# Kernel tuning notes

Measured on AMD Instinct MI355X. Metric: run time of the kernel, lower is better.

Reference implementation:

```python
import jax, jax.numpy as jnp
import numpy as np

N, E, K = 10000, 160000, 5
K3 = K ** 3  # 125 spline kernel entries (kernel_size=5, dim=3)
NUM_CLASSES = 6890
# 8 corner combinations of the degree-1 open B-spline in 3 dims
_COMBOS = jnp.asarray(np.array([[i, j, k] for i in (0, 1) for j in (0, 1) for k in (0, 1)], dtype=np.int32))


def spline_basis(pseudo):
    # pseudo: [E,3] in [0,1]; degree-1 open B-spline, kernel_size K per dim
    p = pseudo * (K - 1)
    lo_f = jnp.floor(p)
    frac = p - lo_f                                   # [E,3]
    lo = jnp.clip(lo_f.astype(jnp.int32), 0, K - 1)    # [E,3]
    hi = jnp.minimum(lo + 1, K - 1)
    w = jnp.stack([1.0 - frac, frac], axis=-1)         # [E,3,2]
    idx = jnp.stack([lo, hi], axis=-1)                 # [E,3,2]
    c = _COMBOS                                        # [8,3]
    b = w[:, 0, c[:, 0]] * w[:, 1, c[:, 1]] * w[:, 2, c[:, 2]]          # [E,8]
    flat = idx[:, 0, c[:, 0]] + K * idx[:, 1, c[:, 1]] + K * K * idx[:, 2, c[:, 2]]  # [E,8]
    return b, flat


def spline_conv(x, src, dst, b, flat, W, root, bias):
    # x: [N,in], W: [K3,in,out], root: [in,out], bias: [out]
    xW = jnp.einsum('ni,kio->nko', x, W)               # [N,K3,out]
    gathered = xW[src[:, None], flat]                  # [E,8,out]
    msg = jnp.einsum('es,eso->eo', b, gathered)        # [E,out]
    agg = jax.ops.segment_sum(msg, dst, num_segments=N)
    deg = jax.ops.segment_sum(jnp.ones((msg.shape[0],), msg.dtype), dst, num_segments=N)
    agg = agg / jnp.maximum(deg, 1.0)[:, None]         # mean aggregation
    return agg + x @ root + bias


def setup_inputs() -> dict:
    key = jax.random.key(0)
    ks = jax.random.split(key, 24)
    s = 0.1
    x = jax.random.normal(ks[0], (N, 1), jnp.float32)
    edge_index = jax.random.randint(ks[1], (2, E), 0, N)
    pseudo = jax.random.uniform(ks[2], (E, 3), dtype=jnp.float32)
    W1 = jax.random.normal(ks[3], (K3, 1, 32), jnp.float32) * s
    root1 = jax.random.normal(ks[4], (1, 32), jnp.float32) * s
    b1 = jnp.zeros((32,), jnp.float32)
    W2 = jax.random.normal(ks[5], (K3, 32, 64), jnp.float32) * s
    root2 = jax.random.normal(ks[6], (32, 64), jnp.float32) * s
    b2 = jnp.zeros((64,), jnp.float32)
    Ws = jax.random.normal(ks[7], (4, K3, 64, 64), jnp.float32) * s  # convs 3-6
    roots = jax.random.normal(ks[8], (4, 64, 64), jnp.float32) * s
    bs = jnp.zeros((4, 64), jnp.float32)
    lin1_w = jax.random.normal(ks[9], (64, 256), jnp.float32) * s
    lin1_b = jnp.zeros((256,), jnp.float32)
    lin2_w = jax.random.normal(ks[10], (256, NUM_CLASSES), jnp.float32) * s
    lin2_b = jnp.zeros((NUM_CLASSES,), jnp.float32)
    return {'x': x, 'edge_index': edge_index, 'pseudo': pseudo,
            'W1': W1, 'root1': root1, 'b1': b1,
            'W2': W2, 'root2': root2, 'b2': b2,
            'Ws': Ws, 'roots': roots, 'bs': bs,
            'lin1_w': lin1_w, 'lin1_b': lin1_b, 'lin2_w': lin2_w, 'lin2_b': lin2_b}


def reference(x, edge_index, pseudo, W1, root1, b1, W2, root2, b2, Ws, roots, bs,
              lin1_w, lin1_b, lin2_w, lin2_b):
    src, dst = edge_index[0], edge_index[1]
    b, flat = spline_basis(pseudo)
    h = jax.nn.elu(spline_conv(x, src, dst, b, flat, W1, root1, b1))
    h = jax.nn.elu(spline_conv(h, src, dst, b, flat, W2, root2, b2))
    for l in range(4):  # convs 3-6, fixed layer loop
        h = jax.nn.elu(spline_conv(h, src, dst, b, flat, Ws[l], roots[l], bs[l]))
    h = jax.nn.elu(h @ lin1_w + lin1_b)
    # dropout is identity in eval mode
    logits = h @ lin2_w + lin2_b
    return jax.nn.log_softmax(logits, axis=-1)
```

## Files before the change

kernel.cpp:

```cpp
#include <hip/hip_runtime.h>
#include <hip/hip_bf16.h>
#include <math.h>

#define Nn 10000
#define Ee 160000
#define NPB 40
#define NBLK 250
#define NKER 125
#define NBUCK (NBLK * NKER)
#define KCHUNK 32

#define MPAD 10048
#define NPAD 6912
#define NCLS 6890

typedef short bf16x8 __attribute__((ext_vector_type(8)));
typedef float f32x4  __attribute__((ext_vector_type(4)));

__global__ __launch_bounds__(256) void basis_kernel(const float* __restrict__ pseudo,
                                                    float* __restrict__ bw,
                                                    int* __restrict__ fl)
{
    int e = blockIdx.x * 256 + threadIdx.x;
    if (e >= Ee) return;
    float p0 = pseudo[e * 3 + 0] * 4.f;
    float p1 = pseudo[e * 3 + 1] * 4.f;
    float p2 = pseudo[e * 3 + 2] * 4.f;
    float f0 = floorf(p0), f1 = floorf(p1), f2 = floorf(p2);
    float fr0 = p0 - f0, fr1 = p1 - f1, fr2 = p2 - f2;
    int lo0 = (int)f0; lo0 = lo0 < 0 ? 0 : (lo0 > 4 ? 4 : lo0);
    int lo1 = (int)f1; lo1 = lo1 < 0 ? 0 : (lo1 > 4 ? 4 : lo1);
    int lo2 = (int)f2; lo2 = lo2 < 0 ? 0 : (lo2 > 4 ? 4 : lo2);
    int hi0 = lo0 + 1 > 4 ? 4 : lo0 + 1;
    int hi1 = lo1 + 1 > 4 ? 4 : lo1 + 1;
    int hi2 = lo2 + 1 > 4 ? 4 : lo2 + 1;
#pragma unroll
    for (int s = 0; s < 8; ++s) {
        int c0 = (s >> 2) & 1, c1 = (s >> 1) & 1, c2 = s & 1;
        float b = (c0 ? fr0 : 1.f - fr0) * (c1 ? fr1 : 1.f - fr1) * (c2 ? fr2 : 1.f - fr2);
        int f = (c0 ? hi0 : lo0) + 5 * (c1 ? hi1 : lo1) + 25 * (c2 ? hi2 : lo2);
        bw[e * 8 + s] = b;
        fl[e * 8 + s] = f;
    }
}

__global__ __launch_bounds__(256) void deg_kernel(const int* __restrict__ dst, int* __restrict__ degi)
{
    int e = blockIdx.x * 256 + threadIdx.x;
    if (e >= Ee) return;
    atomicAdd(&degi[dst[e]], 1);
}

__global__ __launch_bounds__(256) void invdeg_kernel(const int* __restrict__ degi, float* __restrict__ invdeg)
{
    int n = blockIdx.x * 256 + threadIdx.x;
    if (n >= Nn) return;
    int d = degi[n];
    invdeg[n] = 1.f / (float)(d > 0 ? d : 1);
}

__global__ __launch_bounds__(256) void hist_kernel(const int* __restrict__ dst, const int* __restrict__ fl,
                                                   int* __restrict__ hist)
{
    int t = blockIdx.x * 256 + threadIdx.x;
    if (t >= Ee * 8) return;
    int e = t >> 3;
    int key = (dst[e] / NPB) * NKER + fl[t];
    atomicAdd(&hist[key], 1);
}

__global__ __launch_bounds__(1024) void scan_kernel(const int* __restrict__ hist, int* __restrict__ boff)
{
    const int T = 1024;
    const int per = (NBUCK + T - 1) / T;
    int t = threadIdx.x;
    int beg = t * per;
    int end = beg + per; if (end > NBUCK) end = NBUCK;
    int s = 0;
    for (int i = beg; i < end && i < NBUCK; ++i) s += hist[i];
    __shared__ int tmp[1024];
    tmp[t] = s;
    __syncthreads();
    for (int o2 = 1; o2 < 1024; o2 <<= 1) {
        int v = (t >= o2) ? tmp[t - o2] : 0;
        __syncthreads();
        tmp[t] += v;
        __syncthreads();
    }
    int run = tmp[t] - s;
    for (int i = beg; i < end && i < NBUCK; ++i) { boff[i] = run; run += hist[i]; }
    if (t == T - 1) boff[NBUCK] = run;
}

__global__ __launch_bounds__(256) void fill_kernel(const int* __restrict__ srcA, const int* __restrict__ dstA,
                                                   const float* __restrict__ bw, const int* __restrict__ fl,
                                                   int* __restrict__ cursor, uint2* __restrict__ recs)
{
    int t = blockIdx.x * 256 + threadIdx.x;
    if (t >= Ee * 8) return;
    int e = t >> 3;
    int d = dstA[e];
    int key = (d / NPB) * NKER + fl[t];
    int pos = atomicAdd(&cursor[key], 1);
    unsigned meta = (unsigned)srcA[e] | ((unsigned)(d % NPB) << 16);
    recs[pos] = make_uint2(meta, __float_as_uint(bw[t]));
}

template <int CIN, int COUT>
__global__ __launch_bounds__(256) void conv_pairs_kernel(const uint2* __restrict__ recs,
                                                         const int* __restrict__ boff,
                                                         const float* __restrict__ xin,
                                                         const float* __restrict__ W,
                                                         float* __restrict__ agg)
{
    __shared__ float aggl[NPB * COUT];
    const int blk = blockIdx.x;
    for (int idx = threadIdx.x; idx < NPB * COUT; idx += 256) aggl[idx] = 0.f;
    __syncthreads();

    const int lane = threadIdx.x & 63;
    const int wid  = threadIdx.x >> 6;
    const int o    = lane;

    int k0 = blockIdx.y * KCHUNK;
    int k1 = k0 + KCHUNK; if (k1 > NKER) k1 = NKER;

    for (int k = k0 + wid; k < k1; k += 4) {
        int bidx = blk * NKER + k;
        int pb = boff[bidx], pe = boff[bidx + 1];
        if (pb >= pe) continue;
        float wreg[CIN];
#pragma unroll
        for (int i = 0; i < CIN; ++i)
            wreg[i] = (o < COUT) ? W[(k * CIN + i) * COUT + o] : 0.f;

        for (int p = pb; p < pe; ++p) {
            uint2 r = recs[p];
            unsigned meta = (unsigned)__builtin_amdgcn_readfirstlane((int)r.x);
            float wt = __uint_as_float(r.y);
            int src = (int)(meta & 0xFFFFu);
            int dl  = (int)(meta >> 16);
            const float* xs = xin + src * CIN;
            float m0 = 0.f, m1 = 0.f, m2 = 0.f, m3 = 0.f;
            if (CIN >= 4) {
#pragma unroll
                for (int i = 0; i < CIN; i += 4) {
                    m0 += xs[i + 0] * wreg[i + 0];
                    m1 += xs[i + 1] * wreg[i + 1];
                    m2 += xs[i + 2] * wreg[i + 2];
                    m3 += xs[i + 3] * wreg[i + 3];
                }
            } else {
#pragma unroll
                for (int i = 0; i < CIN; ++i) m0 += xs[i] * wreg[i];
            }
            float m = (m0 + m1) + (m2 + m3);
            if (o < COUT) atomicAdd(&aggl[dl * COUT + o], wt * m);
        }
    }
    __syncthreads();
    for (int idx = threadIdx.x; idx < NPB * COUT; idx += 256) {
        int n = blk * NPB + idx / COUT;
        if (n < Nn) atomicAdd(&agg[n * COUT + (idx % COUT)], aggl[idx]);
    }
}

template <int CIN, int COUT>
__global__ __launch_bounds__(256) void epilogue_kernel(const float* __restrict__ agg,
                                                       const float* __restrict__ xin,
                                                       const float* __restrict__ root,
                                                       const float* __restrict__ bias,
                                                       const float* __restrict__ invdeg,
                                                       float* __restrict__ out)
{
    int idx = blockIdx.x * 256 + threadIdx.x;
    int n = idx / COUT, o = idx % COUT;
    if (n >= Nn) return;
    float r0 = 0.f, r1 = 0.f;
#pragma unroll
    for (int i = 0; i < CIN; i += 2) {
        r0 += xin[n * CIN + i] * root[i * COUT + o];
        if (CIN > 1) r1 += xin[n * CIN + i + 1] * root[(i + 1) * COUT + o];
    }
    float v = agg[n * COUT + o] * invdeg[n] + r0 + r1 + bias[o];
    out[n * COUT + o] = v > 0.f ? v : expm1f(v);
}

__global__ __launch_bounds__(256) void lin1_kernel(const float* __restrict__ h,
                                                   const float* __restrict__ w1,
                                                   const float* __restrict__ b1,
                                                   __hip_bfloat16* __restrict__ out)
{
    int n = blockIdx.x;
    __shared__ float hl[64];
    if (threadIdx.x < 64) hl[threadIdx.x] = h[n * 64 + threadIdx.x];
    __syncthreads();
    int j = threadIdx.x;
    float a0 = b1[j], a1 = 0.f, a2 = 0.f, a3 = 0.f;
#pragma unroll
    for (int i = 0; i < 64; i += 4) {
        a0 += hl[i + 0] * w1[(i + 0) * 256 + j];
        a1 += hl[i + 1] * w1[(i + 1) * 256 + j];
        a2 += hl[i + 2] * w1[(i + 2) * 256 + j];
        a3 += hl[i + 3] * w1[(i + 3) * 256 + j];
    }
    float acc = (a0 + a1) + (a2 + a3);
    float v = acc > 0.f ? acc : expm1f(acc);
    out[(size_t)n * 256 + j] = __float2bfloat16(v);
}

__global__ __launch_bounds__(256) void w2t_kernel(const float* __restrict__ w2,
                                                  __hip_bfloat16* __restrict__ w2t)
{
    __shared__ float t[32][33];
    int n0 = blockIdx.x * 32;
    int k0 = blockIdx.y * 32;
    int tx = threadIdx.x & 31, ty = threadIdx.x >> 5;
#pragma unroll
    for (int q = 0; q < 4; ++q) {
        int k = k0 + ty + 8 * q, n = n0 + tx;
        t[ty + 8 * q][tx] = (n < NCLS) ? w2[(size_t)k * NCLS + n] : 0.f;
    }
    __syncthreads();
#pragma unroll
    for (int q = 0; q < 4; ++q) {
        int n = n0 + ty + 8 * q;
        w2t[(size_t)n * 256 + k0 + tx] = __float2bfloat16(t[tx][ty + 8 * q]);
    }
}

__global__ __launch_bounds__(256) void lin2_mfma_kernel(const __hip_bfloat16* __restrict__ hbf,
                                                        const __hip_bfloat16* __restrict__ w2t,
                                                        const float* __restrict__ b2,
                                                        float* __restrict__ out)
{
    const int tid  = threadIdx.x;
    const int lane = tid & 63, wid = tid >> 6;
    const int wr = wid & 1, wc = wid >> 1;
    const int quad = lane >> 4, lq = lane & 15;

    const int mbase = blockIdx.x * 64 + wr * 32;
    const int nbase = blockIdx.y * 128 + wc * 64;

    f32x4 acc[2][4];
#pragma unroll
    for (int i = 0; i < 2; ++i)
#pragma unroll
        for (int j = 0; j < 4; ++j) acc[i][j] = (f32x4){0.f, 0.f, 0.f, 0.f};

    const unsigned short* A = (const unsigned short*)hbf;
    const unsigned short* B = (const unsigned short*)w2t;

    for (int kc = 0; kc < 256; kc += 32) {
        bf16x8 af[2], bfr[4];
#pragma unroll
        for (int mt = 0; mt < 2; ++mt)
            af[mt] = *(const bf16x8*)(A + (size_t)(mbase + mt * 16 + lq) * 256 + kc + quad * 8);
#pragma unroll
        for (int nt = 0; nt < 4; ++nt)
            bfr[nt] = *(const bf16x8*)(B + (size_t)(nbase + nt * 16 + lq) * 256 + kc + quad * 8);
#pragma unroll
        for (int mt = 0; mt < 2; ++mt)
#pragma unroll
            for (int nt = 0; nt < 4; ++nt)
                acc[mt][nt] = __builtin_amdgcn_mfma_f32_16x16x32_bf16(af[mt], bfr[nt], acc[mt][nt], 0, 0, 0);
    }

#pragma unroll
    for (int nt = 0; nt < 4; ++nt) {
        int col = nbase + nt * 16 + lq;
        if (col >= NCLS) continue;
        float bb = b2[col];
#pragma unroll
        for (int mt = 0; mt < 2; ++mt) {
#pragma unroll
            for (int r = 0; r < 4; ++r) {
                int row = mbase + mt * 16 + quad * 4 + r;
                if (row < Nn) out[(size_t)row * NCLS + col] = acc[mt][nt][r] + bb;
            }
        }
    }
}

__global__ __launch_bounds__(1024) void lsm_kernel(float* __restrict__ out)
{
    int row = blockIdx.x;
    float* p = out + (size_t)row * NCLS;
    __shared__ float red[16];
    int tid = threadIdx.x, lane = tid & 63, wid = tid >> 6;

    float m = -3.4e38f;
    for (int jj = tid; jj < NCLS; jj += 1024) m = fmaxf(m, p[jj]);
#pragma unroll
    for (int off = 32; off > 0; off >>= 1) m = fmaxf(m, __shfl_down(m, off));
    if (lane == 0) red[wid] = m;
    __syncthreads();
    if (tid == 0) {
        float mm = red[0];
        for (int w = 1; w < 16; ++w) mm = fmaxf(mm, red[w]);
        red[0] = mm;
    }
    __syncthreads();
    m = red[0];
    __syncthreads();

    float s = 0.f;
    for (int jj = tid; jj < NCLS; jj += 1024) s += expf(p[jj] - m);
#pragma unroll
    for (int off = 32; off > 0; off >>= 1) s += __shfl_down(s, off);
    if (lane == 0) red[wid] = s;
    __syncthreads();
    if (tid == 0) {
        float ss = 0.f;
        for (int w = 1; w < 16; ++w) ss += red[w];
        red[0] += ss;
    }
    __syncthreads();
    float lse = m + logf(red[0]);
    for (int jj = tid; jj < NCLS; jj += 1024) p[jj] -= lse;
}

extern "C" void kernel_launch(void* const* d_in, const int* in_sizes, int n_in,
                              void* d_out, int out_size, void* d_ws, size_t ws_size,
                              hipStream_t stream)
{
    const float* x      = (const float*)d_in[0];
    const int*   ei     = (const int*)d_in[1];
    const float* pseudo = (const float*)d_in[2];
    const float* W1     = (const float*)d_in[3];
    const float* root1  = (const float*)d_in[4];
    const float* b1     = (const float*)d_in[5];
    const float* W2     = (const float*)d_in[6];
    const float* root2  = (const float*)d_in[7];
    const float* b2     = (const float*)d_in[8];
    const float* Ws     = (const float*)d_in[9];
    const float* roots  = (const float*)d_in[10];
    const float* bs     = (const float*)d_in[11];
    const float* l1w    = (const float*)d_in[12];
    const float* l1b    = (const float*)d_in[13];
    const float* l2w    = (const float*)d_in[14];
    const float* l2b    = (const float*)d_in[15];
    float* out = (float*)d_out;

    const int* srcA = ei;
    const int* dstA = ei + Ee;

    char* base = (char*)d_ws;
    size_t off = 0;
    auto carve = [&](size_t bytes) -> void* {
        void* p = base + off;
        off += (bytes + 255) & ~(size_t)255;
        return p;
    };
    float* bw     = (float*)carve((size_t)Ee * 8 * 4);
    int*   fl     = (int*)carve((size_t)Ee * 8 * 4);
    int*   hist   = (int*)carve((size_t)NBUCK * 4);
    int*   boff   = (int*)carve((size_t)(NBUCK + 1) * 4);
    int*   cursor = (int*)carve((size_t)NBUCK * 4);
    uint2* recs   = (uint2*)carve((size_t)Ee * 8 * 8);
    int*   degi   = (int*)carve((size_t)Nn * 4);
    float* invdeg = (float*)carve((size_t)Nn * 4);
    float* agg    = (float*)carve((size_t)Nn * 64 * 4);
    float* hA     = (float*)carve((size_t)Nn * 64 * 4);
    float* hB     = (float*)carve((size_t)Nn * 64 * 4);
    __hip_bfloat16* hbf = (__hip_bfloat16*)carve((size_t)MPAD * 256 * 2);
    __hip_bfloat16* w2t = (__hip_bfloat16*)carve((size_t)NPAD * 256 * 2);
    (void)ws_size; (void)n_in; (void)in_sizes; (void)out_size;

    hipMemsetAsync(hist, 0, (size_t)NBUCK * 4, stream);
    hipMemsetAsync(degi, 0, (size_t)Nn * 4, stream);
    hipMemsetAsync(hbf, 0, (size_t)MPAD * 256 * 2, stream);

    basis_kernel<<<(Ee + 255) / 256, 256, 0, stream>>>(pseudo, bw, fl);
    deg_kernel<<<(Ee + 255) / 256, 256, 0, stream>>>(dstA, degi);
    invdeg_kernel<<<(Nn + 255) / 256, 256, 0, stream>>>(degi, invdeg);
    hist_kernel<<<(Ee * 8 + 255) / 256, 256, 0, stream>>>(dstA, fl, hist);
    scan_kernel<<<1, 1024, 0, stream>>>(hist, boff);
    hipMemcpyAsync(cursor, boff, (size_t)NBUCK * 4, hipMemcpyDeviceToDevice, stream);
    fill_kernel<<<(Ee * 8 + 255) / 256, 256, 0, stream>>>(srcA, dstA, bw, fl, cursor, recs);
    w2t_kernel<<<dim3((NPAD + 31) / 32, 8), 256, 0, stream>>>(l2w, w2t);

    const dim3 cgrid(NBLK, (NKER + KCHUNK - 1) / KCHUNK);

    hipMemsetAsync(agg, 0, (size_t)Nn * 64 * 4, stream);
    conv_pairs_kernel<1, 32><<<cgrid, 256, 0, stream>>>(recs, boff, x, W1, agg);
    epilogue_kernel<1, 32><<<(Nn * 32 + 255) / 256, 256, 0, stream>>>(agg, x, root1, b1, invdeg, hA);

    hipMemsetAsync(agg, 0, (size_t)Nn * 64 * 4, stream);
    conv_pairs_kernel<32, 64><<<cgrid, 256, 0, stream>>>(recs, boff, hA, W2, agg);
    epilogue_kernel<32, 64><<<(Nn * 64 + 255) / 256, 256, 0, stream>>>(agg, hA, root2, b2, invdeg, hB);

    float* cin = hB;
    float* cot = hA;
    for (int l = 0; l < 4; ++l) {
        hipMemsetAsync(agg, 0, (size_t)Nn * 64 * 4, stream);
        conv_pairs_kernel<64, 64><<<cgrid, 256, 0, stream>>>(recs, boff, cin, Ws + (size_t)l * 125 * 64 * 64, agg);
        epilogue_kernel<64, 64><<<(Nn * 64 + 255) / 256, 256, 0, stream>>>(
            agg, cin, roots + (size_t)l * 64 * 64, bs + (size_t)l * 64, invdeg, cot);
        float* t = cin; cin = cot; cot = t;
    }

    lin1_kernel<<<Nn, 256, 0, stream>>>(cin, l1w, l1b, hbf);
    lin2_mfma_kernel<<<dim3(MPAD / 64, NPAD / 128), 256, 0, stream>>>(hbf, w2t, l2b, out);
    lsm_kernel<<<Nn, 1024, 0, stream>>>(out);
}
```

Before: 3.483 ms.

## Restructure spline conv as per-kernel aggregate-then-MFMA with fused epilogue

Replaces the per-edge scalar matvec conv with a scheme that, for each block of 16 destination nodes and each spline kernel entry, first accumulates weighted source features in shared memory. It then multiplies that 16xCIN tile by the transposed bf16 weight slice using MFMA. The root matmul, mean normalisation, bias and ELU are fused into the same kernel, which removes the global agg buffer, its memsets and the separate epilogue. Weights are transposed and cast to bf16 per call, so there is extra prep and precision loss. The scratch buffers bw and fl are reused to hold the transposed weights.

```diff
diff --git a/kernel.cpp b/kernel.cpp
--- a/kernel.cpp
+++ b/kernel.cpp
@@ -4,11 +4,10 @@
 
 #define Nn 10000
 #define Ee 160000
-#define NPB 40
-#define NBLK 250
+#define NPB 16
+#define NBLK 625
 #define NKER 125
 #define NBUCK (NBLK * NKER)
-#define KCHUNK 32
 
 #define MPAD 10048
 #define NPAD 6912
@@ -16,6 +15,11 @@
 
 typedef short bf16x8 __attribute__((ext_vector_type(8)));
 typedef float f32x4  __attribute__((ext_vector_type(4)));
+
+__device__ inline unsigned short f2bf(float f) {
+    unsigned u = __float_as_uint(f);
+    return (unsigned short)((u + 0x7FFFu + ((u >> 16) & 1u)) >> 16);
+}
 
 __global__ __launch_bounds__(256) void basis_kernel(const float* __restrict__ pseudo,
                                                     float* __restrict__ bw,
@@ -65,7 +69,7 @@
     int t = blockIdx.x * 256 + threadIdx.x;
     if (t >= Ee * 8) return;
     int e = t >> 3;
-    int key = (dst[e] / NPB) * NKER + fl[t];
+    int key = (dst[e] >> 4) * NKER + fl[t];
     atomicAdd(&hist[key], 1);
 }
 
@@ -100,90 +104,177 @@
     if (t >= Ee * 8) return;
     int e = t >> 3;
     int d = dstA[e];
-    int key = (d / NPB) * NKER + fl[t];
+    int key = (d >> 4) * NKER + fl[t];
     int pos = atomicAdd(&cursor[key], 1);
-    unsigned meta = (unsigned)srcA[e] | ((unsigned)(d % NPB) << 16);
+    unsigned meta = (unsigned)srcA[e] | ((unsigned)(d & 15) << 16);
     recs[pos] = make_uint2(meta, __float_as_uint(bw[t]));
 }
 
-template <int CIN, int COUT>
-__global__ __launch_bounds__(256) void conv_pairs_kernel(const uint2* __restrict__ recs,
-                                                         const int* __restrict__ boff,
-                                                         const float* __restrict__ xin,
-                                                         const float* __restrict__ W,
-                                                         float* __restrict__ agg)
-{
-    __shared__ float aggl[NPB * COUT];
+__global__ __launch_bounds__(256) void wt_kernel(const float* __restrict__ W,
+                                                 unsigned short* __restrict__ Wt,
+                                                 int CIN, int COUT)
+{
+    __shared__ float t[32][33];
+    int k = blockIdx.x;
+    int nt = COUT / 32;
+    int ti = (blockIdx.y / nt) * 32;
+    int to = (blockIdx.y % nt) * 32;
+    int tx = threadIdx.x & 31, ty = threadIdx.x >> 5;
+    const float* Wk = W + (size_t)k * CIN * COUT;
+    unsigned short* Wtk = Wt + (size_t)k * CIN * COUT;
+#pragma unroll
+    for (int q = 0; q < 4; ++q)
+        t[ty + 8 * q][tx] = Wk[(size_t)(ti + ty + 8 * q) * COUT + to + tx];
+    __syncthreads();
+#pragma unroll
+    for (int q = 0; q < 4; ++q)
+        Wtk[(size_t)(to + ty + 8 * q) * CIN + ti + tx] = f2bf(t[tx][ty + 8 * q]);
+}
+
+__global__ __launch_bounds__(256) void conv1_kernel(const uint2* __restrict__ recs,
+                                                    const int* __restrict__ boff,
+                                                    const float* __restrict__ xin,
+                                                    const float* __restrict__ W1,
+                                                    const float* __restrict__ root1,
+                                                    const float* __restrict__ b1,
+                                                    const float* __restrict__ invdeg,
+                                                    float* __restrict__ out)
+{
+    __shared__ float S[2][16];
+    const int tid = threadIdx.x;
+    const int o = tid & 31, rbase = tid >> 5;
     const int blk = blockIdx.x;
-    for (int idx = threadIdx.x; idx < NPB * COUT; idx += 256) aggl[idx] = 0.f;
-    __syncthreads();
-
-    const int lane = threadIdx.x & 63;
-    const int wid  = threadIdx.x >> 6;
-    const int o    = lane;
-
-    int k0 = blockIdx.y * KCHUNK;
-    int k1 = k0 + KCHUNK; if (k1 > NKER) k1 = NKER;
-
-    for (int k = k0 + wid; k < k1; k += 4) {
-        int bidx = blk * NKER + k;
-        int pb = boff[bidx], pe = boff[bidx + 1];
-        if (pb >= pe) continue;
-        float wreg[CIN];
-#pragma unroll
-        for (int i = 0; i < CIN; ++i)
-            wreg[i] = (o < COUT) ? W[(k * CIN + i) * COUT + o] : 0.f;
-
-        for (int p = pb; p < pe; ++p) {
+    const int kb = blk * NKER;
+
+    float acc0 = 0.f, acc1 = 0.f;
+    if (tid < 32) S[tid >> 4][tid & 15] = 0.f;
+    __syncthreads();
+    int cur = 0;
+    for (int k = 0; k < NKER; ++k) {
+        int pb = boff[kb + k], pe = boff[kb + k + 1];
+        if (pb == pe) continue;
+        for (int p = pb + tid; p < pe; p += 256) {
             uint2 r = recs[p];
-            unsigned meta = (unsigned)__builtin_amdgcn_readfirstlane((int)r.x);
-            float wt = __uint_as_float(r.y);
-            int src = (int)(meta & 0xFFFFu);
-            int dl  = (int)(meta >> 16);
-            const float* xs = xin + src * CIN;
-            float m0 = 0.f, m1 = 0.f, m2 = 0.f, m3 = 0.f;
-            if (CIN >= 4) {
-#pragma unroll
-                for (int i = 0; i < CIN; i += 4) {
-                    m0 += xs[i + 0] * wreg[i + 0];
-                    m1 += xs[i + 1] * wreg[i + 1];
-                    m2 += xs[i + 2] * wreg[i + 2];
-                    m3 += xs[i + 3] * wreg[i + 3];
-                }
-            } else {
-#pragma unroll
-                for (int i = 0; i < CIN; ++i) m0 += xs[i] * wreg[i];
+            int src = (int)(r.x & 0xFFFFu);
+            int dl  = (int)(r.x >> 16);
+            atomicAdd(&S[cur][dl], __uint_as_float(r.y) * xin[src]);
+        }
+        __syncthreads();
+        float w1k = W1[k * 32 + o];
+        acc0 += S[cur][rbase] * w1k;
+        acc1 += S[cur][rbase + 8] * w1k;
+        if (tid < 16) S[cur ^ 1][tid] = 0.f;
+        __syncthreads();
+        cur ^= 1;
+    }
+    int n0 = blk * NPB + rbase;
+    int n1 = n0 + 8;
+    float v0 = acc0 * invdeg[n0] + xin[n0] * root1[o] + b1[o];
+    float v1 = acc1 * invdeg[n1] + xin[n1] * root1[o] + b1[o];
+    out[(size_t)n0 * 32 + o] = v0 > 0.f ? v0 : expm1f(v0);
+    out[(size_t)n1 * 32 + o] = v1 > 0.f ? v1 : expm1f(v1);
+}
+
+template <int CIN>
+__global__ __launch_bounds__(256) void conv_mfma_kernel(const uint2* __restrict__ recs,
+                                                        const int* __restrict__ boff,
+                                                        const float* __restrict__ xin,
+                                                        const unsigned short* __restrict__ Wt,
+                                                        const unsigned short* __restrict__ roott,
+                                                        const float* __restrict__ bias,
+                                                        const float* __restrict__ invdeg,
+                                                        float* __restrict__ out)
+{
+    constexpr int SROW = CIN + 4;
+    __shared__ float S[2][16 * SROW];
+    const int tid = threadIdx.x;
+    const int lane = tid & 63, wid = tid >> 6;
+    const int quad = lane >> 4, lq = lane & 15;
+    const int blk = blockIdx.x;
+    const int kb = blk * NKER;
+
+    f32x4 acc = {0.f, 0.f, 0.f, 0.f};
+
+    for (int idx = tid; idx < 2 * 16 * SROW; idx += 256) ((float*)S)[idx] = 0.f;
+    __syncthreads();
+
+    int cur = 0;
+    for (int k = 0; k < NKER; ++k) {
+        int pb = boff[kb + k], pe = boff[kb + k + 1];
+        if (pb == pe) continue;
+        float* Sc = S[cur];
+        if (CIN == 64) {
+            for (int p = pb + wid; p < pe; p += 4) {
+                uint2 r = recs[p];
+                int src = (int)(r.x & 0xFFFFu);
+                int dl  = (int)(r.x >> 16);
+                float wt = __uint_as_float(r.y);
+                atomicAdd(&Sc[dl * SROW + lane], wt * xin[(size_t)src * CIN + lane]);
             }
-            float m = (m0 + m1) + (m2 + m3);
-            if (o < COUT) atomicAdd(&aggl[dl * COUT + o], wt * m);
+        } else {
+            int half = lane >> 5, feat = lane & 31;
+            for (int p = pb + wid * 2 + half; p < pe; p += 8) {
+                uint2 r = recs[p];
+                int src = (int)(r.x & 0xFFFFu);
+                int dl  = (int)(r.x >> 16);
+                float wt = __uint_as_float(r.y);
+                atomicAdd(&Sc[dl * SROW + feat], wt * xin[(size_t)src * CIN + feat]);
+            }
         }
-    }
-    __syncthreads();
-    for (int idx = threadIdx.x; idx < NPB * COUT; idx += 256) {
-        int n = blk * NPB + idx / COUT;
-        if (n < Nn) atomicAdd(&agg[n * COUT + (idx % COUT)], aggl[idx]);
-    }
-}
-
-template <int CIN, int COUT>
-__global__ __launch_bounds__(256) void epilogue_kernel(const float* __restrict__ agg,
-                                                       const float* __restrict__ xin,
-                                                       const float* __restrict__ root,
-                                                       const float* __restrict__ bias,
-                                                       const float* __restrict__ invdeg,
-                                                       float* __restrict__ out)
-{
-    int idx = blockIdx.x * 256 + threadIdx.x;
-    int n = idx / COUT, o = idx % COUT;
-    if (n >= Nn) return;
-    float r0 = 0.f, r1 = 0.f;
-#pragma unroll
-    for (int i = 0; i < CIN; i += 2) {
-        r0 += xin[n * CIN + i] * root[i * COUT + o];
-        if (CIN > 1) r1 += xin[n * CIN + i + 1] * root[(i + 1) * COUT + o];
-    }
-    float v = agg[n * COUT + o] * invdeg[n] + r0 + r1 + bias[o];
-    out[n * COUT + o] = v > 0.f ? v : expm1f(v);
+        __syncthreads();
+        const unsigned short* Wk = Wt + (size_t)(k * 64 + wid * 16 + lq) * CIN;
+#pragma unroll
+        for (int kc = 0; kc < CIN; kc += 32) {
+            const float* sp = &Sc[lq * SROW + kc + quad * 8];
+            f32x4 a0 = *(const f32x4*)sp;
+            f32x4 a1 = *(const f32x4*)(sp + 4);
+            bf16x8 af;
+            af[0] = (short)f2bf(a0[0]); af[1] = (short)f2bf(a0[1]);
+            af[2] = (short)f2bf(a0[2]); af[3] = (short)f2bf(a0[3]);
+            af[4] = (short)f2bf(a1[0]); af[5] = (short)f2bf(a1[1]);
+            af[6] = (short)f2bf(a1[2]); af[7] = (short)f2bf(a1[3]);
+            bf16x8 bfr = *(const bf16x8*)(Wk + kc + quad * 8);
+            acc = __builtin_amdgcn_mfma_f32_16x16x32_bf16(af, bfr, acc, 0, 0, 0);
+        }
+        float* So = S[cur ^ 1];
+        for (int idx = tid; idx < 16 * SROW; idx += 256) So[idx] = 0.f;
+        __syncthreads();
+        cur ^= 1;
+    }
+
+#pragma unroll
+    for (int r = 0; r < 4; ++r)
+        acc[r] *= invdeg[blk * NPB + quad * 4 + r];
+
+    float* Sc = S[cur];
+    for (int idx = tid; idx < 16 * CIN; idx += 256) {
+        int row = idx / CIN, i = idx - row * CIN;
+        Sc[row * SROW + i] = xin[(size_t)(blk * NPB + row) * CIN + i];
+    }
+    __syncthreads();
+    const unsigned short* Rk = roott + (size_t)(wid * 16 + lq) * CIN;
+#pragma unroll
+    for (int kc = 0; kc < CIN; kc += 32) {
+        const float* sp = &Sc[lq * SROW + kc + quad * 8];
+        f32x4 a0 = *(const f32x4*)sp;
+        f32x4 a1 = *(const f32x4*)(sp + 4);
+        bf16x8 af;
+        af[0] = (short)f2bf(a0[0]); af[1] = (short)f2bf(a0[1]);
+        af[2] = (short)f2bf(a0[2]); af[3] = (short)f2bf(a0[3]);
+        af[4] = (short)f2bf(a1[0]); af[5] = (short)f2bf(a1[1]);
+        af[6] = (short)f2bf(a1[2]); af[7] = (short)f2bf(a1[3]);
+        bf16x8 bfr = *(const bf16x8*)(Rk + kc + quad * 8);
+        acc = __builtin_amdgcn_mfma_f32_16x16x32_bf16(af, bfr, acc, 0, 0, 0);
+    }
+
+    int col = wid * 16 + lq;
+    float bb = bias[col];
+#pragma unroll
+    for (int r = 0; r < 4; ++r) {
+        int n = blk * NPB + quad * 4 + r;
+        float v = acc[r] + bb;
+        out[(size_t)n * 64 + col] = v > 0.f ? v : expm1f(v);
+    }
 }
 
 __global__ __launch_bounds__(256) void lin1_kernel(const float* __restrict__ h,
@@ -360,12 +451,16 @@
     uint2* recs   = (uint2*)carve((size_t)Ee * 8 * 8);
     int*   degi   = (int*)carve((size_t)Nn * 4);
     float* invdeg = (float*)carve((size_t)Nn * 4);
-    float* agg    = (float*)carve((size_t)Nn * 64 * 4);
     float* hA     = (float*)carve((size_t)Nn * 64 * 4);
     float* hB     = (float*)carve((size_t)Nn * 64 * 4);
     __hip_bfloat16* hbf = (__hip_bfloat16*)carve((size_t)MPAD * 256 * 2);
     __hip_bfloat16* w2t = (__hip_bfloat16*)carve((size_t)NPAD * 256 * 2);
     (void)ws_size; (void)n_in; (void)in_sizes; (void)out_size;
+
+    unsigned short* W2t    = (unsigned short*)bw;
+    unsigned short* root2t = (unsigned short*)((char*)bw + 524288);
+    unsigned short* rootst = (unsigned short*)((char*)bw + 532480);
+    unsigned short* Wst    = (unsigned short*)fl;
 
     hipMemsetAsync(hist, 0, (size_t)NBUCK * 4, stream);
     hipMemsetAsync(degi, 0, (size_t)Nn * 4, stream);
@@ -378,25 +473,28 @@
     scan_kernel<<<1, 1024, 0, stream>>>(hist, boff);
     hipMemcpyAsync(cursor, boff, (size_t)NBUCK * 4, hipMemcpyDeviceToDevice, stream);
     fill_kernel<<<(Ee * 8 + 255) / 256, 256, 0, stream>>>(srcA, dstA, bw, fl, cursor, recs);
+
     w2t_kernel<<<dim3((NPAD + 31) / 32, 8), 256, 0, stream>>>(l2w, w2t);
-
-    const dim3 cgrid(NBLK, (NKER + KCHUNK - 1) / KCHUNK);
-
-    hipMemsetAsync(agg, 0, (size_t)Nn * 64 * 4, stream);
-    conv_pairs_kernel<1, 32><<<cgrid, 256, 0, stream>>>(recs, boff, x, W1, agg);
-    epilogue_kernel<1, 32><<<(Nn * 32 + 255) / 256, 256, 0, stream>>>(agg, x, root1, b1, invdeg, hA);
-
-    hipMemsetAsync(agg, 0, (size_t)Nn * 64 * 4, stream);
-    conv_pairs_kernel<32, 64><<<cgrid, 256, 0, stream>>>(recs, boff, hA, W2, agg);
-    epilogue_kernel<32, 64><<<(Nn * 64 + 255) / 256, 256, 0, stream>>>(agg, hA, root2, b2, invdeg, hB);
+    wt_kernel<<<dim3(125, 2), 256, 0, stream>>>(W2, W2t, 32, 64);
+    wt_kernel<<<dim3(1, 2), 256, 0, stream>>>(root2, root2t, 32, 64);
+    for (int l = 0; l < 4; ++l) {
+        wt_kernel<<<dim3(125, 4), 256, 0, stream>>>(Ws + (size_t)l * 125 * 64 * 64,
+                                                    Wst + (size_t)l * 125 * 64 * 64, 64, 64);
+        wt_kernel<<<dim3(1, 4), 256, 0, stream>>>(roots + (size_t)l * 64 * 64,
+                                                  rootst + (size_t)l * 64 * 64, 64, 64);
+    }
+
+    conv1_kernel<<<NBLK, 256, 0, stream>>>(recs, boff, x, W1, root1, b1, invdeg, hA);
+
+    conv_mfma_kernel<32><<<NBLK, 256, 0, stream>>>(recs, boff, hA, W2t, root2t, b2, invdeg, hB);
 
     float* cin = hB;
     float* cot = hA;
     for (int l = 0; l < 4; ++l) {
-        hipMemsetAsync(agg, 0, (size_t)Nn * 64 * 4, stream);
-        conv_pairs_kernel<64, 64><<<cgrid, 256, 0, stream>>>(recs, boff, cin, Ws + (size_t)l * 125 * 64 * 64, agg);
-        epilogue_kernel<64, 64><<<(Nn * 64 + 255) / 256, 256, 0, stream>>>(
-            agg, cin, roots + (size_t)l * 64 * 64, bs + (size_t)l * 64, invdeg, cot);
+        conv_mfma_kernel<64><<<NBLK, 256, 0, stream>>>(recs, boff, cin,
+                                                       Wst + (size_t)l * 125 * 64 * 64,
+                                                       rootst + (size_t)l * 64 * 64,
+                                                       bs + (size_t)l * 64, invdeg, cot);
         float* t = cin; cin = cot; cot = t;
     }
 
```

Measured after the change: 3.892 ms. 11.7% more time.
